# Optimization experiments

Measured on AMD Instinct MI355X. Metric: run time of the kernel, lower is better.

## Reference

```python
import jax, jax.numpy as jnp
import numpy as np

D_MODEL = 1024
N_HEADS = 16
D_KV = 64
INNER = N_HEADS * D_KV  # 1024


def setup_inputs() -> dict:
    key = jax.random.key(0)
    ks = jax.random.split(key, 6)
    B, SV, ST = 4, 1024, 1024
    vis = jax.random.normal(ks[0], (B, SV, D_MODEL), dtype=jnp.float32)
    txt = jax.random.normal(ks[1], (B, ST, D_MODEL), dtype=jnp.float32)
    s = 0.02
    Wq = jax.random.normal(ks[2], (D_MODEL, INNER), dtype=jnp.float32) * s
    Wk = jax.random.normal(ks[3], (D_MODEL, INNER), dtype=jnp.float32) * s
    Wv = jax.random.normal(ks[4], (D_MODEL, INNER), dtype=jnp.float32) * s
    Wo = jax.random.normal(ks[5], (INNER, D_MODEL), dtype=jnp.float32) * s
    return {"vis_hidden_states": vis, "txt_hidden_states": txt,
            "Wq": Wq, "Wk": Wk, "Wv": Wv, "Wo": Wo}


def _split_heads(x):
    # [B, S, INNER] -> [B, H, S, Dk]
    B, S, _ = x.shape
    return x.reshape(B, S, N_HEADS, D_KV).transpose(0, 2, 1, 3)


def _merge_heads(x):
    # [B, H, S, Dk] -> [B, S, INNER]
    B, H, S, Dk = x.shape
    return x.transpose(0, 2, 1, 3).reshape(B, S, H * Dk)


def reference(vis_hidden_states, txt_hidden_states, Wq, Wk, Wv, Wo):
    # T5-style attention: NO 1/sqrt(d) scaling, no biases.
    q = _split_heads(vis_hidden_states @ Wq)   # [B,H,Sv,Dk]
    k = _split_heads(txt_hidden_states @ Wk)   # [B,H,St,Dk]
    v = _split_heads(txt_hidden_states @ Wv)   # [B,H,St,Dk]
    v2 = _split_heads(vis_hidden_states @ Wv)  # [B,H,Sv,Dk]

    scores = jnp.einsum('bhqd,bhkd->bhqk', q, k)  # [B,H,Sv,St]
    attn = jax.nn.softmax(scores.astype(jnp.float32), axis=-1).astype(scores.dtype)

    vis_out = jnp.einsum('bhqk,bhkd->bhqd', attn, v)   # softmax-normalized over k
    txt_out = jnp.einsum('bhqk,bhqd->bhkd', attn, v2)  # transposed attn, NOT renormalized

    vis_out = _merge_heads(vis_out) @ Wo  # [B,Sv,D]
    txt_out = _merge_heads(txt_out) @ Wo  # [B,St,D]
    return vis_out, txt_out
```

## Files before the change

### kernel.cpp

```cpp
#include <hip/hip_runtime.h>

typedef unsigned short u16;
typedef unsigned int u32;
typedef __bf16 bf16x8 __attribute__((ext_vector_type(8)));
typedef float f32x4 __attribute__((ext_vector_type(4)));
typedef u16 u16x4 __attribute__((ext_vector_type(4)));
typedef __attribute__((address_space(1))) void* as1_t;
typedef __attribute__((address_space(3))) void* as3_t;

#define LOG2E 1.4426950408889634f
#define MFMA(a,b,c) __builtin_amdgcn_mfma_f32_16x16x32_bf16(a,b,c,0,0,0)

__device__ __forceinline__ u16 f2bf(float f){
  u32 u = __float_as_uint(f);
  return (u16)((u + 0x7FFFu + ((u >> 16) & 1u)) >> 16);
}
__device__ __forceinline__ float bf2f(u16 x){
  return __uint_as_float(((u32)x) << 16);
}
#if __has_builtin(__builtin_amdgcn_cvt_pk_bf16_f32)
__device__ __forceinline__ u16x4 pk4(float a, float b, float c, float d){
  auto lo = __builtin_amdgcn_cvt_pk_bf16_f32(a,b);
  auto hi = __builtin_amdgcn_cvt_pk_bf16_f32(c,d);
  union { u16x4 v; u32 w[2]; } u;
  u.w[0] = __builtin_bit_cast(u32, lo);
  u.w[1] = __builtin_bit_cast(u32, hi);
  return u.v;
}
#else
__device__ __forceinline__ u16x4 pk4(float a, float b, float c, float d){
  u16x4 r = { f2bf(a), f2bf(b), f2bf(c), f2bf(d) };
  return r;
}
#endif
__device__ __forceinline__ void gld16(const u16* gp, u16* lp){
  __builtin_amdgcn_global_load_lds((as1_t)(u16*)gp, (as3_t)lp, 16, 0, 0);
}

#define SBAR  __builtin_amdgcn_s_barrier()
#define SCHB  __builtin_amdgcn_sched_barrier(0)
#define SP1   __builtin_amdgcn_s_setprio(1)
#define SP0   __builtin_amdgcn_s_setprio(0)
#define WAITL0 asm volatile("s_waitcnt lgkmcnt(0)" ::: "memory")
#define WAITV6 asm volatile("s_waitcnt vmcnt(6)" ::: "memory")
#define WAITV8 asm volatile("s_waitcnt vmcnt(8)" ::: "memory")

__global__ void prep_kernel(const float* __restrict__ vis, u16* __restrict__ vis16,
                            const float* __restrict__ txt, u16* __restrict__ txt16,
                            const float* __restrict__ Wq, const float* __restrict__ Wk,
                            const float* __restrict__ Wv, const float* __restrict__ Wo,
                            u16* __restrict__ T0, u16* __restrict__ T1,
                            u16* __restrict__ T2, u16* __restrict__ T3,
                            u16* __restrict__ T4){
  int bid = blockIdx.x;
  if(bid < 8192){
    const float* src = (bid < 4096) ? vis : txt;
    u16* dst = (bid < 4096) ? vis16 : txt16;
    int idx = ((bid & 4095)*256 + threadIdx.x)*4;
    float4 v = *(const float4*)(src + idx);
    *(u16x4*)(dst + idx) = pk4(v.x, v.y, v.z, v.w);
    return;
  }
  int rr = bid - 8192;
  int wi = rr >> 8, tile = rr & 255;
  const float* W; u16* WT;
  switch(wi){
    case 0: W = Wq; WT = T0; break;
    case 1: W = Wv; WT = T1; break;
    case 2: W = Wk; WT = T2; break;
    case 3: W = Wv; WT = T3; break;
    default: W = Wo; WT = T4; break;
  }
  __shared__ u16 t[64][65];
  int bn = (tile & 15)*64, bk = (tile >> 4)*64;
  int c = threadIdx.x & 63, r0 = threadIdx.x >> 6;
  #pragma unroll
  for(int j=0;j<64;j+=4){
    int r = r0 + j;
    t[r][c] = f2bf(W[(bk + r)*1024 + bn + c]);
  }
  __syncthreads();
  #pragma unroll
  for(int j=0;j<64;j+=4){
    int r = r0 + j;
    WT[(bn + r)*1024 + bk + c] = t[c][r];
  }
}

__global__ __launch_bounds__(512, 2)
void proj_gemm_kernel(const u16* __restrict__ Avis, const u16* __restrict__ Atxt,
                      const u16* __restrict__ Wvis, const u16* __restrict__ Wtxt,
                      u16* __restrict__ Qb, u16* __restrict__ V2t,
                      u16* __restrict__ Kb, u16* __restrict__ Vt)
{
  const u16 *A, *Bt; u16 *Cn, *Ct;
  if(blockIdx.z == 0){ A = Avis; Bt = Wvis; Cn = Qb; Ct = V2t; }
  else               { A = Atxt; Bt = Wtxt; Cn = Kb; Ct = Vt;  }
  __shared__ u16 lds[65536];
  const int tid = threadIdx.x, w = tid >> 6, lane = tid & 63;
  const int quad = lane >> 4, cl = lane & 15;
  const int wr = w >> 2, wc = w & 3;
  const int bm = blockIdx.x*256, bn = blockIdx.y*256;
  const int sx0 = ((quad    ) ^ (cl & 7)) << 3;
  const int sx1 = ((quad + 4) ^ (cl & 7)) << 3;
  const int arow = ((wr << 7) + cl) << 6;
  const int brow = (((wc << 6) + cl) << 6) + 16384;

  f32x4 acc[8][4];
  #pragma unroll
  for(int a=0;a<8;a++)
    #pragma unroll
    for(int b=0;b<4;b++){ f32x4 z = {0.f,0.f,0.f,0.f}; acc[a][b] = z; }
  bf16x8 af[4][2], bfv0[2][2], bfv1[2][2];

#define STG(G, gbase, dsto, kk) { \
    _Pragma("unroll") \
    for(int ii=0;ii<4;ii++){ \
      int slot_ = ii*512 + tid; int r_ = slot_ >> 3, cs_ = slot_ & 7; \
      gld16((G) + (size_t)((gbase) + r_)*1024 + (kk) + ((cs_ ^ (r_ & 7)) << 3), \
            lds + (dsto) + (ii*512 + (w << 6))*8); } }

#define LDA_(bo, mh) { \
    _Pragma("unroll") \
    for(int q_=0;q_<4;q_++){ \
      int ro_ = (bo) + arow + (((mh)*4 + q_) << 10); \
      af[q_][0] = *(const bf16x8*)(lds + ro_ + sx0); \
      af[q_][1] = *(const bf16x8*)(lds + ro_ + sx1); } }

#define LDB_(bo, nh, bfv) { \
    _Pragma("unroll") \
    for(int j_=0;j_<2;j_++){ \
      int ro_ = (bo) + brow + (((nh)*2 + j_) << 10); \
      bfv[j_][0] = *(const bf16x8*)(lds + ro_ + sx0); \
      bfv[j_][1] = *(const bf16x8*)(lds + ro_ + sx1); } }

#define MM_(mh, bfv, nh) { \
    _Pragma("unroll") \
    for(int q_=0;q_<4;q_++) \
      _Pragma("unroll") \
      for(int j_=0;j_<2;j_++){ \
        acc[(mh)*4+q_][(nh)*2+j_] = MFMA(af[q_][0], bfv[j_][0], acc[(mh)*4+q_][(nh)*2+j_]); \
        acc[(mh)*4+q_][(nh)*2+j_] = MFMA(af[q_][1], bfv[j_][1], acc[(mh)*4+q_][(nh)*2+j_]); } }

#define TILE(bufo, ts) { \
    LDA_(bufo, 0); LDB_(bufo, 0, bfv0); \
    SBAR; WAITL0; SCHB; SP1; MM_(0, bfv0, 0); SP0; SBAR; \
    LDB_(bufo, 1, bfv1); \
    SBAR; WAITL0; SCHB; SP1; MM_(0, bfv1, 1); SP0; SBAR; \
    LDA_(bufo, 1); \
    SBAR; WAITL0; SCHB; SP1; MM_(1, bfv1, 1); SP0; SBAR; \
    STG(A , bm, (bufo)        , ts); \
    STG(Bt, bn, (bufo) + 16384, ts); \
    SCHB; SP1; MM_(1, bfv0, 0); SP0; \
    WAITV8; SBAR; }

  STG(A , bm, 0,     0);  STG(Bt, bn, 16384, 0);
  STG(A , bm, 32768, 64); STG(Bt, bn, 32768+16384, 64);
  WAITV8; SBAR;

  for(int tt=0; tt<8; tt++){
    const int t0 = 2*tt;
    TILE(0,     ((t0+2)&15) << 6);
    TILE(32768, ((t0+3)&15) << 6);
  }
#undef STG
#undef LDA_
#undef LDB_
#undef MM_
#undef TILE

  if(bn < 1024){
    #pragma unroll
    for(int mf=0; mf<8; mf++){
      int m0 = bm + wr*128 + mf*16 + quad*4;
      #pragma unroll
      for(int nf=0; nf<4; nf++){
        int n = bn + wc*64 + nf*16 + cl;
        int h = n >> 6, d = n & 63;
        #pragma unroll
        for(int i2=0;i2<4;i2++){
          int m = m0 + i2; int b = m >> 10, s = m & 1023;
          Cn[(((size_t)(b*16 + h)*1024 + s) << 6) + d] = f2bf(acc[mf][nf][i2]);
        }
      }
    }
  } else {
    #pragma unroll
    for(int mf=0; mf<8; mf++){
      int m0 = bm + wr*128 + mf*16 + quad*4;
      int b = m0 >> 10, s = m0 & 1023;
      #pragma unroll
      for(int nf=0; nf<4; nf++){
        int nn = bn - 1024 + wc*64 + nf*16 + cl;
        int h = nn >> 6, d = nn & 63;
        *(u16x4*)(Ct + (((size_t)(b*16 + h)*64 + d) << 10) + s) =
            pk4(acc[mf][nf][0], acc[mf][nf][1], acc[mf][nf][2], acc[mf][nf][3]);
      }
    }
  }
}

__device__ __forceinline__ void gemm_pipe(const u16* __restrict__ A,
                                          const u16* __restrict__ Bt,
                                          int bm, int bn,
                                          u16* __restrict__ lds,
                                          f32x4 (&acc)[4][4],
                                          int tid, int w, int quad, int cl,
                                          int wr, int wc)
{
  const int sx0 = ((quad    ) ^ (cl & 7)) << 3;
  const int sx1 = ((quad + 4) ^ (cl & 7)) << 3;
  const int arow = ((wr << 6) + cl) << 6;
  const int brow = (((wc << 6) + cl) << 6) + 16384;
  bf16x8 af[4][2], bfv[2][2];

#define STAGE128(G, gbase, dsto, kk) { \
    _Pragma("unroll") \
    for(int ii=0;ii<2;ii++){ \
      int slot_ = ii*512 + tid; int r_ = slot_ >> 3, cs_ = slot_ & 7; \
      gld16((G) + (size_t)((gbase) + r_)*1024 + (kk) + ((cs_ ^ (r_ & 7)) << 3), \
            lds + (dsto) + (ii*512 + (w << 6))*8); } }

#define LDA_(bo) { \
    _Pragma("unroll") \
    for(int m_=0;m_<4;m_++){ \
      int ro_ = (bo) + arow + (m_ << 10); \
      af[m_][0] = *(const bf16x8*)(lds + ro_ + sx0); \
      af[m_][1] = *(const bf16x8*)(lds + ro_ + sx1); } }

#define LDB_(bo, nh) { \
    _Pragma("unroll") \
    for(int j_=0;j_<2;j_++){ \
      int ro_ = (bo) + brow + (((nh)*2 + j_) << 10); \
      bfv[j_][0] = *(const bf16x8*)(lds + ro_ + sx0); \
      bfv[j_][1] = *(const bf16x8*)(lds + ro_ + sx1); } }

#define MM_(nh) { \
    _Pragma("unroll") \
    for(int m_=0;m_<4;m_++) \
      _Pragma("unroll") \
      for(int j_=0;j_<2;j_++){ \
        acc[m_][(nh)*2+j_] = MFMA(af[m_][0], bfv[j_][0], acc[m_][(nh)*2+j_]); \
        acc[m_][(nh)*2+j_] = MFMA(af[m_][1], bfv[j_][1], acc[m_][(nh)*2+j_]); } }

  STAGE128(A , bm      , 0,          0);
  STAGE128(A , bm + 128, 8192,       0);
  STAGE128(Bt, bn      , 16384,      0);
  STAGE128(A , bm      , 24576,      64);
  STAGE128(A , bm + 128, 24576+8192, 64);
  STAGE128(Bt, bn      , 24576+16384,64);
  WAITV6; SBAR;

  #pragma unroll 2
  for(int t=0;t<16;t++){
    const int c  = (t % 3) * 24576;
    const int n2 = ((t+2) % 3) * 24576;
    const int ts = ((t+2) & 15) << 6;
    LDA_(c); LDB_(c, 0);
    STAGE128(A, bm      , n2,        ts);
    STAGE128(A, bm + 128, n2 + 8192, ts);
    SBAR; WAITL0; SCHB;
    SP1; MM_(0); SP0;
    SBAR;
    LDB_(c, 1);
    STAGE128(Bt, bn, n2 + 16384, ts);
    SBAR; WAITL0; SCHB;
    SP1; MM_(1); SP0;
    WAITV6;
    SBAR;
  }
#undef STAGE128
#undef LDA_
#undef LDB_
#undef MM_
}

__global__ __launch_bounds__(512, 2)
void out_gemm_kernel(const u16* __restrict__ A, const u16* __restrict__ Bt,
                     float* __restrict__ Cf)
{
  __shared__ u16 lds[73728];
  const int tid = threadIdx.x, w = tid >> 6, lane = tid & 63;
  const int quad = lane >> 4, cl = lane & 15;
  const int wr = w >> 1, wc = w & 1;
  const int bm = blockIdx.x*256, bn = blockIdx.y*128;

  f32x4 acc[4][4];
  #pragma unroll
  for(int a=0;a<4;a++)
    #pragma unroll
    for(int b=0;b<4;b++){ f32x4 z = {0.f,0.f,0.f,0.f}; acc[a][b] = z; }

  gemm_pipe(A, Bt, bm, bn, lds, acc, tid, w, quad, cl, wr, wc);

  #pragma unroll
  for(int mf=0; mf<4; mf++)
    #pragma unroll
    for(int nf=0; nf<4; nf++)
      #pragma unroll
      for(int i=0;i<4;i++){
        int m = bm + wr*64 + mf*16 + quad*4 + i;
        int n = bn + wc*64 + nf*16 + cl;
        Cf[(size_t)m*1024 + n] = acc[mf][nf][i];
      }
}

__global__ __launch_bounds__(512, 4)
void attn_vis_kernel(const u16* __restrict__ Q, const u16* __restrict__ Kc,
                     const u16* __restrict__ Vt, u16* __restrict__ visA,
                     float* __restrict__ rl_g)
{
  __shared__ u16 lds[17408];
  u16* Pl  = lds;
  u16* Kst = lds + 9216;
  u16* Vst = lds + 13312;
  const int tid = threadIdx.x, w = tid>>6, lane = tid&63;
  const int quad = lane>>4, cl = lane&15;
  const int bh = blockIdx.x, q0 = blockIdx.y*128;
  const u16* Qh  = Q  + (size_t)bh*65536;
  const u16* Kh  = Kc + (size_t)bh*65536;
  const u16* Vth = Vt + (size_t)bh*65536;

  #pragma unroll
  for(int i=0;i<2;i++){
    int slot = i*512 + tid;
    int c = slot >> 7, r = slot & 127;
    gld16(Qh + (size_t)(q0 + r)*64 + c*8, Pl + slot*8);
  }
  __syncthreads();
  bf16x8 qf[2];
  #pragma unroll
  for(int kk=0;kk<2;kk++)
    qf[kk] = *(const bf16x8*)(Pl + ((kk*4+quad)*128 + w*16 + cl)*8);
  __syncthreads();

  float lrun = 0.f;
  f32x4 oacc[4];
  #pragma unroll
  for(int dt=0;dt<4;dt++){ f32x4 z = {0.f,0.f,0.f,0.f}; oacc[dt] = z; }

  for(int kt=0;kt<16;kt++){
    __syncthreads();
    {
      int slot = tid;
      { int c = slot >> 6, r = slot & 63;
        gld16(Kh + (size_t)(kt*64 + r)*64 + c*8, Kst + slot*8); }
      { int d = slot >> 3, ch = slot & 7;
        gld16(Vth + (size_t)d*1024 + kt*64 + (ch^(d&7))*8, Vst + slot*8); }
    }
    __syncthreads();
    #pragma unroll
    for(int mtk=0;mtk<4;mtk++){
      f32x4 s = {0.f,0.f,0.f,0.f};
      #pragma unroll
      for(int kk=0;kk<2;kk++){
        bf16x8 ka = *(const bf16x8*)(Kst + ((kk*4+quad)*64 + mtk*16 + cl)*8);
        s = MFMA(ka, qf[kk], s);
      }
      float p0 = __builtin_amdgcn_exp2f(s[0]*LOG2E);
      float p1 = __builtin_amdgcn_exp2f(s[1]*LOG2E);
      float p2 = __builtin_amdgcn_exp2f(s[2]*LOG2E);
      float p3 = __builtin_amdgcn_exp2f(s[3]*LOG2E);
      lrun += (p0+p1)+(p2+p3);
      *(u16x4*)(Pl + (w*16 + cl)*72 + mtk*16 + quad*4) = pk4(p0,p1,p2,p3);
    }
    bf16x8 pa[2];
    #pragma unroll
    for(int kk=0;kk<2;kk++)
      pa[kk] = *(const bf16x8*)(Pl + (w*16 + cl)*72 + kk*32 + quad*8);
    #pragma unroll
    for(int dt=0;dt<4;dt++){
      int d = dt*16 + cl;
      #pragma unroll
      for(int kk=0;kk<2;kk++){
        bf16x8 vb = *(const bf16x8*)(Vst + d*64 + (((kk*4+quad)^(d&7))*8));
        oacc[dt] = MFMA(pa[kk], vb, oacc[dt]);
      }
    }
  }
  lrun += __shfl_xor(lrun, 16, 64);
  lrun += __shfl_xor(lrun, 32, 64);
  float rl = 1.f/lrun;
  if(quad == 0) rl_g[bh*1024 + q0 + w*16 + cl] = rl;
  const int b = bh >> 4, h = bh & 15;
  #pragma unroll
  for(int i=0;i<4;i++){
    float rr = __shfl(rl, quad*4 + i, 16);
    int q = q0 + w*16 + quad*4 + i;
    #pragma unroll
    for(int dt=0;dt<4;dt++)
      visA[(size_t)(b*1024 + q)*1024 + h*64 + dt*16 + cl] = f2bf(oacc[dt][i]*rr);
  }
}

__global__ __launch_bounds__(512, 4)
void attn_txt_kernel(const u16* __restrict__ Kc, const u16* __restrict__ Q,
                     const u16* __restrict__ V2t, const float* __restrict__ rl_g,
                     u16* __restrict__ txtA)
{
  __shared__ u16 lds[17408];
  u16* Pl  = lds;
  u16* Qst = lds + 9216;
  u16* Vst = lds + 13312;
  const int tid = threadIdx.x, w = tid>>6, lane = tid&63;
  const int quad = lane>>4, cl = lane&15;
  const int bh = blockIdx.x, k0 = blockIdx.y*128;
  const u16* Kh  = Kc  + (size_t)bh*65536;
  const u16* Qh  = Q   + (size_t)bh*65536;
  const u16* Vth = V2t + (size_t)bh*65536;

  #pragma unroll
  for(int i=0;i<2;i++){
    int slot = i*512 + tid;
    int c = slot >> 7, r = slot & 127;
    gld16(Kh + (size_t)(k0 + r)*64 + c*8, Pl + slot*8);
  }
  __syncthreads();
  bf16x8 kb[2];
  #pragma unroll
  for(int kk=0;kk<2;kk++)
    kb[kk] = *(const bf16x8*)(Pl + ((kk*4+quad)*128 + w*16 + cl)*8);
  __syncthreads();

  f32x4 oacc[4];
  #pragma unroll
  for(int dt=0;dt<4;dt++){ f32x4 z = {0.f,0.f,0.f,0.f}; oacc[dt] = z; }

  for(int qt=0;qt<16;qt++){
    __syncthreads();
    {
      int slot = tid;
      { int c = slot >> 6, r = slot & 63;
        gld16(Qh + (size_t)(qt*64 + r)*64 + c*8, Qst + slot*8); }
      { int d = slot >> 3, ch = slot & 7;
        gld16(Vth + (size_t)d*1024 + qt*64 + (ch^(d&7))*8, Vst + slot*8); }
    }
    __syncthreads();
    f32x4 rv[4];
    #pragma unroll
    for(int mtq=0;mtq<4;mtq++)
      rv[mtq] = *(const f32x4*)(rl_g + bh*1024 + qt*64 + mtq*16 + quad*4);
    #pragma unroll
    for(int mtq=0;mtq<4;mtq++){
      f32x4 s = {0.f,0.f,0.f,0.f};
      #pragma unroll
      for(int kk=0;kk<2;kk++){
        bf16x8 qa = *(const bf16x8*)(Qst + ((kk*4+quad)*64 + mtq*16 + cl)*8);
        s = MFMA(qa, kb[kk], s);
      }
      float p0 = __builtin_amdgcn_exp2f(s[0]*LOG2E)*rv[mtq][0];
      float p1 = __builtin_amdgcn_exp2f(s[1]*LOG2E)*rv[mtq][1];
      float p2 = __builtin_amdgcn_exp2f(s[2]*LOG2E)*rv[mtq][2];
      float p3 = __builtin_amdgcn_exp2f(s[3]*LOG2E)*rv[mtq][3];
      *(u16x4*)(Pl + (w*16 + cl)*72 + mtq*16 + quad*4) = pk4(p0,p1,p2,p3);
    }
    bf16x8 pa[2];
    #pragma unroll
    for(int kk=0;kk<2;kk++)
      pa[kk] = *(const bf16x8*)(Pl + (w*16 + cl)*72 + kk*32 + quad*8);
    #pragma unroll
    for(int dt=0;dt<4;dt++){
      int d = dt*16 + cl;
      #pragma unroll
      for(int kk=0;kk<2;kk++){
        bf16x8 vb = *(const bf16x8*)(Vst + d*64 + (((kk*4+quad)^(d&7))*8));
        oacc[dt] = MFMA(pa[kk], vb, oacc[dt]);
      }
    }
  }
  const int b = bh >> 4, h = bh & 15;
  #pragma unroll
  for(int i=0;i<4;i++){
    int k = k0 + w*16 + quad*4 + i;
    #pragma unroll
    for(int dt=0;dt<4;dt++)
      txtA[(size_t)(b*1024 + k)*1024 + h*64 + dt*16 + cl] = f2bf(oacc[dt][i]);
  }
}

extern "C" void kernel_launch(void* const* d_in, const int* in_sizes, int n_in,
                              void* d_out, int out_size, void* d_ws, size_t ws_size,
                              hipStream_t stream)
{
  const float* vis = (const float*)d_in[0];
  const float* txt = (const float*)d_in[1];
  const float* Wq  = (const float*)d_in[2];
  const float* Wk  = (const float*)d_in[3];
  const float* Wv  = (const float*)d_in[4];
  const float* Wo  = (const float*)d_in[5];
  float* out = (float*)d_out;

  char* ws = (char*)d_ws;
  const size_t MB = 1u << 20;
  u16* vis16 = (u16*)(ws + 0);
  u16* txt16 = (u16*)(ws + 8*MB);
  u16* Wvis  = (u16*)(ws + 16*MB);
  u16* Wtxt  = (u16*)(ws + 20*MB);
  u16* Qb    = (u16*)(ws + 24*MB);
  u16* Kb    = (u16*)(ws + 32*MB);
  u16* Vt    = (u16*)(ws + 40*MB);
  u16* V2t   = (u16*)(ws + 48*MB);
  float* rl_g = (float*)(ws + 56*MB);
  u16* WoT   = (u16*)(ws + 57*MB);
  u16* visA = vis16;  u16* txtA = txt16;

  prep_kernel<<<9472, 256, 0, stream>>>(vis, vis16, txt, txt16,
                                        Wq, Wk, Wv, Wo,
                                        Wvis, Wvis + 1048576, Wtxt, Wtxt + 1048576, WoT);
  proj_gemm_kernel<<<dim3(16,8,2), 512, 0, stream>>>(vis16, txt16, Wvis, Wtxt,
                                                     Qb, V2t, Kb, Vt);
  attn_vis_kernel<<<dim3(64,8), 512, 0, stream>>>(Qb, Kb, Vt, visA, rl_g);
  attn_txt_kernel<<<dim3(64,8), 512, 0, stream>>>(Kb, Qb, V2t, rl_g, txtA);
  out_gemm_kernel<<<dim3(32,8), 512, 0, stream>>>(visA, WoT, out);
}
```

Before: 223.2 us.

## Restructure projection GEMM main loop into split-half staged pipeline

Rewrites the projection GEMM mainloop so each 64-wide K tile of A and B is staged in two halves. The half-tile global-to-LDS loads are interleaved with the four MFMA quadrants, using finer vmcnt waits. A separate af0/af1 fragment set lets the next tile's first A fragments load during the current tile, and the LDS row layout is remapped so each half holds contiguous fragment rows. The aim is to hide global load latency and cut barrier stalls. In exchange it adds registers and more complex wait counting, with an explicit epilogue for the last tile.

```diff
diff --git a/kernel.cpp b/kernel.cpp
--- a/kernel.cpp
+++ b/kernel.cpp
@@ -43,7 +43,9 @@
 #define SP0   __builtin_amdgcn_s_setprio(0)
 #define WAITL0 asm volatile("s_waitcnt lgkmcnt(0)" ::: "memory")
 #define WAITV6 asm volatile("s_waitcnt vmcnt(6)" ::: "memory")
-#define WAITV8 asm volatile("s_waitcnt vmcnt(8)" ::: "memory")
+#define WV0 asm volatile("s_waitcnt vmcnt(0)" ::: "memory")
+#define WV2 asm volatile("s_waitcnt vmcnt(2)" ::: "memory")
+#define WV4 asm volatile("s_waitcnt vmcnt(4)" ::: "memory")
 
 __global__ void prep_kernel(const float* __restrict__ vis, u16* __restrict__ vis16,
                             const float* __restrict__ txt, u16* __restrict__ txt16,
@@ -103,71 +105,99 @@
   const int bm = blockIdx.x*256, bn = blockIdx.y*256;
   const int sx0 = ((quad    ) ^ (cl & 7)) << 3;
   const int sx1 = ((quad + 4) ^ (cl & 7)) << 3;
-  const int arow = ((wr << 7) + cl) << 6;
-  const int brow = (((wc << 6) + cl) << 6) + 16384;
+  const int arow = ((wr << 6) + cl) << 6;
+  const int brow = (((wc << 5) + cl) << 6) + 16384;
 
   f32x4 acc[8][4];
   #pragma unroll
   for(int a=0;a<8;a++)
     #pragma unroll
     for(int b=0;b<4;b++){ f32x4 z = {0.f,0.f,0.f,0.f}; acc[a][b] = z; }
-  bf16x8 af[4][2], bfv0[2][2], bfv1[2][2];
-
-#define STG(G, gbase, dsto, kk) { \
-    _Pragma("unroll") \
-    for(int ii=0;ii<4;ii++){ \
+  bf16x8 af0[4][2], af1[4][2], bfv0[2][2], bfv1[2][2];
+
+#define STGA(gbase, bufo, h, kk) { \
+    _Pragma("unroll") \
+    for(int ii=0;ii<2;ii++){ \
       int slot_ = ii*512 + tid; int r_ = slot_ >> 3, cs_ = slot_ & 7; \
-      gld16((G) + (size_t)((gbase) + r_)*1024 + (kk) + ((cs_ ^ (r_ & 7)) << 3), \
-            lds + (dsto) + (ii*512 + (w << 6))*8); } }
-
-#define LDA_(bo, mh) { \
+      int gr_ = (h)*64 + (r_ & 63) + ((r_ >> 6) << 7); \
+      gld16(A + (size_t)((gbase) + gr_)*1024 + (kk) + ((cs_ ^ (r_ & 7)) << 3), \
+            lds + (bufo) + (h)*8192 + (ii*512 + (w << 6))*8); } }
+#define STGB(gbase, bufo, h, kk) { \
+    _Pragma("unroll") \
+    for(int ii=0;ii<2;ii++){ \
+      int slot_ = ii*512 + tid; int r_ = slot_ >> 3, cs_ = slot_ & 7; \
+      int gr_ = ((r_ >> 5) << 6) + (h)*32 + (r_ & 31); \
+      gld16(Bt + (size_t)((gbase) + gr_)*1024 + (kk) + ((cs_ ^ (r_ & 7)) << 3), \
+            lds + (bufo) + 16384 + (h)*8192 + (ii*512 + (w << 6))*8); } }
+
+#define LDA_(bo, mh, dst) { \
     _Pragma("unroll") \
     for(int q_=0;q_<4;q_++){ \
-      int ro_ = (bo) + arow + (((mh)*4 + q_) << 10); \
-      af[q_][0] = *(const bf16x8*)(lds + ro_ + sx0); \
-      af[q_][1] = *(const bf16x8*)(lds + ro_ + sx1); } }
-
-#define LDB_(bo, nh, bfv) { \
+      int ro_ = (bo) + (mh)*8192 + arow + (q_ << 10); \
+      dst[q_][0] = *(const bf16x8*)(lds + ro_ + sx0); \
+      dst[q_][1] = *(const bf16x8*)(lds + ro_ + sx1); } }
+
+#define LDB_(bo, nh, dst) { \
     _Pragma("unroll") \
     for(int j_=0;j_<2;j_++){ \
-      int ro_ = (bo) + brow + (((nh)*2 + j_) << 10); \
-      bfv[j_][0] = *(const bf16x8*)(lds + ro_ + sx0); \
-      bfv[j_][1] = *(const bf16x8*)(lds + ro_ + sx1); } }
-
-#define MM_(mh, bfv, nh) { \
+      int ro_ = (bo) + (nh)*8192 + brow + (j_ << 10); \
+      dst[j_][0] = *(const bf16x8*)(lds + ro_ + sx0); \
+      dst[j_][1] = *(const bf16x8*)(lds + ro_ + sx1); } }
+
+#define MM_(a_, b_, mh, nh) { \
     _Pragma("unroll") \
     for(int q_=0;q_<4;q_++) \
       _Pragma("unroll") \
       for(int j_=0;j_<2;j_++){ \
-        acc[(mh)*4+q_][(nh)*2+j_] = MFMA(af[q_][0], bfv[j_][0], acc[(mh)*4+q_][(nh)*2+j_]); \
-        acc[(mh)*4+q_][(nh)*2+j_] = MFMA(af[q_][1], bfv[j_][1], acc[(mh)*4+q_][(nh)*2+j_]); } }
-
-#define TILE(bufo, ts) { \
-    LDA_(bufo, 0); LDB_(bufo, 0, bfv0); \
-    SBAR; WAITL0; SCHB; SP1; MM_(0, bfv0, 0); SP0; SBAR; \
-    LDB_(bufo, 1, bfv1); \
-    SBAR; WAITL0; SCHB; SP1; MM_(0, bfv1, 1); SP0; SBAR; \
-    LDA_(bufo, 1); \
-    SBAR; WAITL0; SCHB; SP1; MM_(1, bfv1, 1); SP0; SBAR; \
-    STG(A , bm, (bufo)        , ts); \
-    STG(Bt, bn, (bufo) + 16384, ts); \
-    SCHB; SP1; MM_(1, bfv0, 0); SP0; \
-    WAITV8; SBAR; }
-
-  STG(A , bm, 0,     0);  STG(Bt, bn, 16384, 0);
-  STG(A , bm, 32768, 64); STG(Bt, bn, 32768+16384, 64);
-  WAITV8; SBAR;
-
-  for(int tt=0; tt<8; tt++){
-    const int t0 = 2*tt;
-    TILE(0,     ((t0+2)&15) << 6);
-    TILE(32768, ((t0+3)&15) << 6);
-  }
-#undef STG
+        acc[(mh)*4+q_][(nh)*2+j_] = MFMA(a_[q_][0], b_[j_][0], acc[(mh)*4+q_][(nh)*2+j_]); \
+        acc[(mh)*4+q_][(nh)*2+j_] = MFMA(a_[q_][1], b_[j_][1], acc[(mh)*4+q_][(nh)*2+j_]); } }
+
+  STGA(bm, 0, 0, 0);
+  STGB(bn, 0, 0, 0);
+  STGB(bn, 0, 1, 0);
+  WV4;
+  SBAR;
+  LDA_(0, 0, af0);
+  STGA(bm, 0, 1, 0);
+  WV2;
+
+  #pragma unroll 2
+  for(int t=0; t<15; ++t){
+    const int c  = (t & 1) << 15;
+    const int nb = ((t+1) & 1) << 15;
+    const int ts = (t+1) << 6;
+    SBAR;
+    LDB_(c, 0, bfv0); LDB_(c, 1, bfv1);
+    STGA(bm, nb, 0, ts);
+    SP1; MM_(af0, bfv0, 0, 0); SP0;
+    WV2;
+    SBAR;
+    LDA_(c, 1, af1);
+    STGB(bn, nb, 0, ts);
+    SP1; MM_(af0, bfv1, 0, 1); SP0;
+    SBAR;
+    STGB(bn, nb, 1, ts);
+    SP1; MM_(af1, bfv1, 1, 1); SP0;
+    WV4;
+    SBAR;
+    LDA_(nb, 0, af0);
+    STGA(bm, nb, 1, ts);
+    SP1; MM_(af1, bfv0, 1, 0); SP0;
+    WV2;
+  }
+  WV0;
+  SBAR;
+  LDB_(32768, 0, bfv0); LDB_(32768, 1, bfv1);
+  LDA_(32768, 1, af1);
+  MM_(af0, bfv0, 0, 0);
+  MM_(af0, bfv1, 0, 1);
+  MM_(af1, bfv1, 1, 1);
+  MM_(af1, bfv0, 1, 0);
+#undef STGA
+#undef STGB
 #undef LDA_
 #undef LDB_
 #undef MM_
-#undef TILE
 
   if(bn < 1024){
     #pragma unroll
```

Measured after the change: 239.3 us. 1.07x slower.
